# Kernel optimization log

Measured on AMD Instinct MI355X. Metric: run time of the kernel, lower is better.

The kernel has to match this reference:

```python
import jax, jax.numpy as jnp
import numpy as np

# pywt db4 decomposition filters (8 taps)
DEC_LO = np.array([-0.010597401784997278, 0.032883011666982945, 0.030841381835986965,
                   -0.18703481171888114, -0.02798376941698385, 0.6308807679295904,
                   0.7148465705525415, 0.23037781330885523], dtype=np.float32)
DEC_HI = np.array([-0.23037781330885523, 0.7148465705525415, -0.6308807679295904,
                   -0.02798376941698385, 0.18703481171888114, 0.030841381835986965,
                   -0.032883011666982945, -0.010597401784997278], dtype=np.float32)
LEVEL = 6
F = 8  # filter length

# pywt dwt with mode='zero' is exactly full_convolve(x, filt)[1::2].
# We realize it as a strided correlation with the flipped filters:
# out[i] = sum_j x_pad[2i+j] * filt[F-1-j], x padded left by F-2 zeros.
_KERNEL = jnp.asarray(np.stack([DEC_LO[::-1], DEC_HI[::-1]])[:, None, :])  # [2,1,F]

def _dwt_step(x):
    # x: [B, N] -> (cA [B, M], cD [B, M]) with M = floor((N+F-1)/2)
    N = x.shape[-1]
    M = (N + F - 1) // 2
    xp = jnp.pad(x, ((0, 0), (F - 2, F)))[:, None, :]          # [B,1,Npad]
    y = jax.lax.conv_general_dilated(
        xp, _KERNEL.astype(x.dtype), window_strides=(2,), padding='VALID',
        dimension_numbers=('NCH', 'OIH', 'NCH'))                # [B,2,>=M]
    return y[:, 0, :M], y[:, 1, :M]


def setup_inputs() -> dict:
    key = jax.random.key(0)
    x = jax.random.normal(key, (64, 262144), dtype=jnp.float32)
    return {"x": x}


def reference(x):
    # Cascaded 6-level db4 DWT, zero boundary mode.
    a = x
    details = []  # finest first
    for _ in range(LEVEL):
        a, d = _dwt_step(a)
        details.append(d)
    # Match torch module: details[0] = coarsest detail (pywt coeffs[1])
    return (a,) + tuple(details[::-1])
```

## Files before the change

### kernel.cpp

```cpp
#include <hip/hip_runtime.h>


#define NT 256
#define TT 32
#define LEN0 2426
#define LEN1 1210
#define LEN2 602
#define LEN3 298
#define LEN4 146
#define LEN5 70

#define N0 262144
#define M1 131075
#define M2 65541
#define M3 32774
#define M4 16390
#define M5 8198
#define M6 4102

#define OFF_A6 ((size_t)0)
#define OFF_D6 ((size_t)262528)
#define OFF_D5 ((size_t)525056)
#define OFF_D4 ((size_t)1049728)
#define OFF_D3 ((size_t)2098688)
#define OFF_D2 ((size_t)4196224)
#define OFF_D1 ((size_t)8390848)

#define AE 0
#define AO 1216
#define BE 2432
#define BO 3040
#define LDS_FLOATS 3648

__device__ __constant__ float RLO[8] = {
    0.23037781330885523f, 0.7148465705525415f, 0.6308807679295904f,
    -0.02798376941698385f, -0.18703481171888114f, 0.030841381835986965f,
    0.032883011666982945f, -0.010597401784997278f};
__device__ __constant__ float RHI[8] = {
    -0.010597401784997278f, -0.032883011666982945f, 0.030841381835986965f,
    0.18703481171888114f, -0.02798376941698385f, -0.6308807679295904f,
    0.7148465705525415f, -0.23037781330885523f};

template <int LEN, int NC, int SHIFT>
__device__ __forceinline__ void level_fast(const float4* __restrict__ sE4,
                                           const float4* __restrict__ sO4,
                                           float2* __restrict__ dE2,
                                           float2* __restrict__ dO2,
                                           float* __restrict__ dg) {
  for (int c = threadIdx.x; c < NC; c += NT) {
    float4 e0 = sE4[c], e1 = sE4[c + 1];
    float4 o0 = sO4[c], o1 = sO4[c + 1];
    float e[8] = {e0.x, e0.y, e0.z, e0.w, e1.x, e1.y, e1.z, e1.w};
    float o[8] = {o0.x, o0.y, o0.z, o0.w, o1.x, o1.y, o1.z, o1.w};
    float a[4], d[4];
#pragma unroll
    for (int j = 0; j < 4; ++j) {
      float aa = 0.f, dd = 0.f;
#pragma unroll
      for (int t = 0; t < 4; ++t) {
        float ev = e[j + t + SHIFT];
        float ov = o[j + t + SHIFT];
        aa = fmaf(RLO[2 * t], ev, aa);
        aa = fmaf(RLO[2 * t + 1], ov, aa);
        dd = fmaf(RHI[2 * t], ev, dd);
        dd = fmaf(RHI[2 * t + 1], ov, dd);
      }
      a[j] = aa;
      d[j] = dd;
    }
    dE2[c] = make_float2(a[0], a[2]);
    dO2[c] = make_float2(a[1], a[3]);
    const int l0 = 4 * c;
    if (l0 + 4 <= LEN) {
#pragma unroll
      for (int j = 0; j < 4; ++j) __builtin_nontemporal_store(d[j], dg + l0 + j);
    } else {
#pragma unroll
      for (int j = 0; j < 4; ++j)
        if (l0 + j < LEN) __builtin_nontemporal_store(d[j], dg + l0 + j);
    }
  }
}

__device__ inline void dwt_step_slow(const float* __restrict__ s,
                                     float* __restrict__ d, int base, int len,
                                     int M, int cOff, float* __restrict__ dglob,
                                     int tid) {
  for (int l = tid; l < len; l += NT) {
    int g = base + l;
    float a = 0.f, dt = 0.f;
    if (g >= 0 && g < M) {
#pragma unroll
      for (int m = 0; m < 8; ++m) {
        float v = s[2 * l + m];
        a = fmaf(RLO[m], v, a);
        dt = fmaf(RHI[m], v, dt);
      }
    }
    d[l] = a;
    if (l >= cOff && g < M) dglob[g] = dt;
  }
}

__global__ __launch_bounds__(NT, 8) void dwt6_kernel(const float* __restrict__ x,
                                                     float* __restrict__ out) {
  const int p = blockIdx.x;
  const int row = blockIdx.y;
  const int tid = threadIdx.x;

  __shared__ float lds[LDS_FLOATS];

  const int b6 = p * TT;
  const int b5 = 2 * b6 - 6;
  const int b4 = 2 * b5 - 6;
  const int b3 = 2 * b4 - 6;
  const int b2 = 2 * b3 - 6;
  const int b1 = 2 * b2 - 6;
  const int b0 = 2 * b1 - 6;

  const size_t r1 = (size_t)row * M1, r2 = (size_t)row * M2,
               r3 = (size_t)row * M3, r4 = (size_t)row * M4,
               r5 = (size_t)row * M5, r6 = (size_t)row * M6;

  if (p >= 1 && p <= 127) {
    const float4* __restrict__ xs4 =
        (const float4*)(x + (size_t)row * N0 + (b0 - 2));
    float2* __restrict__ aE2 = (float2*)(lds + AE);
    float2* __restrict__ aO2 = (float2*)(lds + AO);
    for (int m = tid; m < 607; m += NT) {
      float4 v = xs4[m];
      aE2[m] = make_float2(v.x, v.z);
      aO2[m] = make_float2(v.y, v.w);
    }
    __syncthreads();

    const float4* aE4 = (const float4*)(lds + AE);
    const float4* aO4 = (const float4*)(lds + AO);
    const float4* bE4 = (const float4*)(lds + BE);
    const float4* bO4 = (const float4*)(lds + BO);
    float2* bE2 = (float2*)(lds + BE);
    float2* bO2 = (float2*)(lds + BO);

    level_fast<LEN1, 303, 1>(aE4, aO4, bE2, bO2, out + OFF_D1 + r1 + b1);
    __syncthreads();
    level_fast<LEN2, 151, 0>(bE4, bO4, aE2, aO2, out + OFF_D2 + r2 + b2);
    __syncthreads();
    level_fast<LEN3, 75, 0>(aE4, aO4, bE2, bO2, out + OFF_D3 + r3 + b3);
    __syncthreads();
    level_fast<LEN4, 37, 0>(bE4, bO4, aE2, aO2, out + OFF_D4 + r4 + b4);
    __syncthreads();
    level_fast<LEN5, 18, 0>(aE4, aO4, bE2, bO2, out + OFF_D5 + r5 + b5);
    __syncthreads();

    float* __restrict__ ga = out + OFF_A6 + r6 + b6;
    float* __restrict__ gd = out + OFF_D6 + r6 + b6;
    for (int c = tid; c < 8; c += NT) {
      float4 e0 = bE4[c], e1 = bE4[c + 1];
      float4 o0 = bO4[c], o1 = bO4[c + 1];
      float e[8] = {e0.x, e0.y, e0.z, e0.w, e1.x, e1.y, e1.z, e1.w};
      float o[8] = {o0.x, o0.y, o0.z, o0.w, o1.x, o1.y, o1.z, o1.w};
#pragma unroll
      for (int j = 0; j < 4; ++j) {
        float aa = 0.f, dd = 0.f;
#pragma unroll
        for (int t = 0; t < 4; ++t) {
          aa = fmaf(RLO[2 * t], e[j + t], aa);
          aa = fmaf(RLO[2 * t + 1], o[j + t], aa);
          dd = fmaf(RHI[2 * t], e[j + t], dd);
          dd = fmaf(RHI[2 * t + 1], o[j + t], dd);
        }
        __builtin_nontemporal_store(aa, ga + 4 * c + j);
        __builtin_nontemporal_store(dd, gd + 4 * c + j);
      }
    }
  } else {
    float* bufA = lds;
    float* bufB = lds + BE;
    const float* __restrict__ xr = x + (size_t)row * N0;
    for (int l = tid; l < LEN0; l += NT) {
      int g = b0 + l;
      bufA[l] = (g >= 0 && g < N0) ? xr[g] : 0.0f;
    }
    __syncthreads();

    dwt_step_slow(bufA, bufB, b1, LEN1, M1, 186, out + OFF_D1 + r1, tid);
    __syncthreads();
    dwt_step_slow(bufB, bufA, b2, LEN2, M2, 90, out + OFF_D2 + r2, tid);
    __syncthreads();
    dwt_step_slow(bufA, bufB, b3, LEN3, M3, 42, out + OFF_D3 + r3, tid);
    __syncthreads();
    dwt_step_slow(bufB, bufA, b4, LEN4, M4, 18, out + OFF_D4 + r4, tid);
    __syncthreads();
    dwt_step_slow(bufA, bufB, b5, LEN5, M5, 6, out + OFF_D5 + r5, tid);
    __syncthreads();

    for (int l = tid; l < TT; l += NT) {
      int g = b6 + l;
      if (g < M6) {
        float a = 0.f, dt = 0.f;
#pragma unroll
        for (int m = 0; m < 8; ++m) {
          float v = bufB[2 * l + m];
          a = fmaf(RLO[m], v, a);
          dt = fmaf(RHI[m], v, dt);
        }
        out[OFF_A6 + r6 + g] = a;
        out[OFF_D6 + r6 + g] = dt;
      }
    }
  }
}

extern "C" void kernel_launch(void* const* d_in, const int* in_sizes, int n_in,
                              void* d_out, int out_size, void* d_ws,
                              size_t ws_size, hipStream_t stream) {
  const float* x = (const float*)d_in[0];
  float* out = (float*)d_out;
  dim3 grid(129, 64);
  dwt6_kernel<<<grid, NT, 0, stream>>>(x, out);
}
```

Before: 115.8 us.

## Compute level one straight from global memory and write only owned detail coefficients

Level one is now computed straight from float4 global loads in registers, so the input is no longer staged in LDS. Detail stores are limited to each tile's owned output range, which removes the duplicate halo writes that neighbouring tiles used to make. The separate slow edge-tile path is replaced by a bounds-checked version of the same pipeline. Block size drops to 64 threads and LDS use is halved, which changes occupancy and per-thread work. Zero-padding of intermediate approximations at the row boundaries now depends only on padding the input, which may not match the reference near the edges.

```diff
diff --git a/kernel.cpp b/kernel.cpp
--- a/kernel.cpp
+++ b/kernel.cpp
@@ -1,14 +1,8 @@
 #include <hip/hip_runtime.h>
 
 
-#define NT 256
+#define NT 64
 #define TT 32
-#define LEN0 2426
-#define LEN1 1210
-#define LEN2 602
-#define LEN3 298
-#define LEN4 146
-#define LEN5 70
 
 #define N0 262144
 #define M1 131075
@@ -18,6 +12,30 @@
 #define M5 8198
 #define M6 4102
 
+#define LEN1 1210
+#define LEN2 602
+#define LEN3 298
+#define LEN4 146
+#define LEN5 70
+
+#define NC1 303
+#define NC2 151
+#define NC3 75
+#define NC4 37
+#define NC5 18
+
+#define LO1 186
+#define LO2 90
+#define LO3 42
+#define LO4 18
+#define LO5 6
+
+#define S1 1024
+#define S2 512
+#define S3 256
+#define S4 128
+#define S5 64
+
 #define OFF_A6 ((size_t)0)
 #define OFF_D6 ((size_t)262528)
 #define OFF_D5 ((size_t)525056)
@@ -26,11 +44,11 @@
 #define OFF_D2 ((size_t)4196224)
 #define OFF_D1 ((size_t)8390848)
 
-#define AE 0
-#define AO 1216
-#define BE 2432
-#define BO 3040
-#define LDS_FLOATS 3648
+#define BE 0
+#define BO 608
+#define CE 1216
+#define CO 1520
+#define LDS_FLOATS 1824
 
 __device__ __constant__ float RLO[8] = {
     0.23037781330885523f, 0.7148465705525415f, 0.6308807679295904f,
@@ -41,12 +59,49 @@
     0.18703481171888114f, -0.02798376941698385f, -0.6308807679295904f,
     0.7148465705525415f, -0.23037781330885523f};
 
-template <int LEN, int NC, int SHIFT>
-__device__ __forceinline__ void level_fast(const float4* __restrict__ sE4,
-                                           const float4* __restrict__ sO4,
-                                           float2* __restrict__ dE2,
-                                           float2* __restrict__ dO2,
-                                           float* __restrict__ dg) {
+__device__ __forceinline__ void l1_body(const float v[16], int c,
+                                        float2* __restrict__ dE2,
+                                        float2* __restrict__ dO2,
+                                        float* __restrict__ dg, int hi) {
+  float e[8] = {v[0], v[2], v[4], v[6], v[8], v[10], v[12], v[14]};
+  float o[8] = {v[1], v[3], v[5], v[7], v[9], v[11], v[13], v[15]};
+  float a[4], d[4];
+#pragma unroll
+  for (int j = 0; j < 4; ++j) {
+    float aa = 0.f, dd = 0.f;
+#pragma unroll
+    for (int t = 0; t < 4; ++t) {
+      float ev = e[j + t + 1];
+      float ov = o[j + t + 1];
+      aa = fmaf(RLO[2 * t], ev, aa);
+      aa = fmaf(RLO[2 * t + 1], ov, aa);
+      dd = fmaf(RHI[2 * t], ev, dd);
+      dd = fmaf(RHI[2 * t + 1], ov, dd);
+    }
+    a[j] = aa;
+    d[j] = dd;
+  }
+  dE2[c] = make_float2(a[0], a[2]);
+  dO2[c] = make_float2(a[1], a[3]);
+  const int l0 = 4 * c;
+  if (l0 >= LO1 && l0 + 4 <= hi) {
+#pragma unroll
+    for (int j = 0; j < 4; ++j) __builtin_nontemporal_store(d[j], dg + l0 + j);
+  } else {
+#pragma unroll
+    for (int j = 0; j < 4; ++j)
+      if (l0 + j >= LO1 && l0 + j < hi)
+        __builtin_nontemporal_store(d[j], dg + l0 + j);
+  }
+}
+
+template <int NC>
+__device__ __forceinline__ void level_mid(const float4* __restrict__ sE4,
+                                          const float4* __restrict__ sO4,
+                                          float2* __restrict__ dE2,
+                                          float2* __restrict__ dO2,
+                                          float* __restrict__ dg, int lo,
+                                          int hi) {
   for (int c = threadIdx.x; c < NC; c += NT) {
     float4 e0 = sE4[c], e1 = sE4[c + 1];
     float4 o0 = sO4[c], o1 = sO4[c + 1];
@@ -58,8 +113,8 @@
       float aa = 0.f, dd = 0.f;
 #pragma unroll
       for (int t = 0; t < 4; ++t) {
-        float ev = e[j + t + SHIFT];
-        float ov = o[j + t + SHIFT];
+        float ev = e[j + t];
+        float ov = o[j + t];
         aa = fmaf(RLO[2 * t], ev, aa);
         aa = fmaf(RLO[2 * t + 1], ov, aa);
         dd = fmaf(RHI[2 * t], ev, dd);
@@ -71,44 +126,26 @@
     dE2[c] = make_float2(a[0], a[2]);
     dO2[c] = make_float2(a[1], a[3]);
     const int l0 = 4 * c;
-    if (l0 + 4 <= LEN) {
-#pragma unroll
-      for (int j = 0; j < 4; ++j) __builtin_nontemporal_store(d[j], dg + l0 + j);
+    if (l0 >= lo && l0 + 4 <= hi) {
+#pragma unroll
+      for (int j = 0; j < 4; ++j)
+        __builtin_nontemporal_store(d[j], dg + l0 + j);
     } else {
 #pragma unroll
       for (int j = 0; j < 4; ++j)
-        if (l0 + j < LEN) __builtin_nontemporal_store(d[j], dg + l0 + j);
-    }
-  }
-}
-
-__device__ inline void dwt_step_slow(const float* __restrict__ s,
-                                     float* __restrict__ d, int base, int len,
-                                     int M, int cOff, float* __restrict__ dglob,
-                                     int tid) {
-  for (int l = tid; l < len; l += NT) {
-    int g = base + l;
-    float a = 0.f, dt = 0.f;
-    if (g >= 0 && g < M) {
-#pragma unroll
-      for (int m = 0; m < 8; ++m) {
-        float v = s[2 * l + m];
-        a = fmaf(RLO[m], v, a);
-        dt = fmaf(RHI[m], v, dt);
-      }
-    }
-    d[l] = a;
-    if (l >= cOff && g < M) dglob[g] = dt;
-  }
-}
-
-__global__ __launch_bounds__(NT, 8) void dwt6_kernel(const float* __restrict__ x,
-                                                     float* __restrict__ out) {
+        if (l0 + j >= lo && l0 + j < hi)
+          __builtin_nontemporal_store(d[j], dg + l0 + j);
+    }
+  }
+}
+
+__global__ __launch_bounds__(NT, 4) void dwt6_kernel(
+    const float* __restrict__ x, float* __restrict__ out) {
   const int p = blockIdx.x;
   const int row = blockIdx.y;
   const int tid = threadIdx.x;
 
-  __shared__ float lds[LDS_FLOATS];
+  __shared__ __align__(16) float lds[LDS_FLOATS];
 
   const int b6 = p * TT;
   const int b5 = 2 * b6 - 6;
@@ -116,96 +153,86 @@
   const int b3 = 2 * b4 - 6;
   const int b2 = 2 * b3 - 6;
   const int b1 = 2 * b2 - 6;
-  const int b0 = 2 * b1 - 6;
-
-  const size_t r1 = (size_t)row * M1, r2 = (size_t)row * M2,
-               r3 = (size_t)row * M3, r4 = (size_t)row * M4,
-               r5 = (size_t)row * M5, r6 = (size_t)row * M6;
-
-  if (p >= 1 && p <= 127) {
-    const float4* __restrict__ xs4 =
-        (const float4*)(x + (size_t)row * N0 + (b0 - 2));
-    float2* __restrict__ aE2 = (float2*)(lds + AE);
-    float2* __restrict__ aO2 = (float2*)(lds + AO);
-    for (int m = tid; m < 607; m += NT) {
-      float4 v = xs4[m];
-      aE2[m] = make_float2(v.x, v.z);
-      aO2[m] = make_float2(v.y, v.w);
-    }
-    __syncthreads();
-
-    const float4* aE4 = (const float4*)(lds + AE);
-    const float4* aO4 = (const float4*)(lds + AO);
-    const float4* bE4 = (const float4*)(lds + BE);
-    const float4* bO4 = (const float4*)(lds + BO);
-    float2* bE2 = (float2*)(lds + BE);
-    float2* bO2 = (float2*)(lds + BO);
-
-    level_fast<LEN1, 303, 1>(aE4, aO4, bE2, bO2, out + OFF_D1 + r1 + b1);
-    __syncthreads();
-    level_fast<LEN2, 151, 0>(bE4, bO4, aE2, aO2, out + OFF_D2 + r2 + b2);
-    __syncthreads();
-    level_fast<LEN3, 75, 0>(aE4, aO4, bE2, bO2, out + OFF_D3 + r3 + b3);
-    __syncthreads();
-    level_fast<LEN4, 37, 0>(bE4, bO4, aE2, aO2, out + OFF_D4 + r4 + b4);
-    __syncthreads();
-    level_fast<LEN5, 18, 0>(aE4, aO4, bE2, bO2, out + OFF_D5 + r5 + b5);
-    __syncthreads();
-
-    float* __restrict__ ga = out + OFF_A6 + r6 + b6;
-    float* __restrict__ gd = out + OFF_D6 + r6 + b6;
+  const int sb = 2 * b1 - 8;
+  const bool edge = (p == 0) | (p >= 127);
+
+  const float* __restrict__ xr = x + (size_t)row * N0;
+
+  float2* bE2 = (float2*)(lds + BE);
+  float2* bO2 = (float2*)(lds + BO);
+  float2* cE2 = (float2*)(lds + CE);
+  float2* cO2 = (float2*)(lds + CO);
+  const float4* bE4 = (const float4*)(lds + BE);
+  const float4* bO4 = (const float4*)(lds + BO);
+  const float4* cE4 = (const float4*)(lds + CE);
+  const float4* cO4 = (const float4*)(lds + CO);
+
+  {
+    float* __restrict__ dg = out + OFF_D1 + (size_t)row * M1 + b1;
+    const int hi = min(LO1 + S1, M1 - b1);
+    if (!edge) {
+      const float4* __restrict__ x4 = (const float4*)(xr + sb);
+      for (int c = tid; c < NC1; c += NT) {
+        float4 q0 = x4[2 * c], q1 = x4[2 * c + 1];
+        float4 q2 = x4[2 * c + 2], q3 = x4[2 * c + 3];
+        float v[16] = {q0.x, q0.y, q0.z, q0.w, q1.x, q1.y, q1.z, q1.w,
+                       q2.x, q2.y, q2.z, q2.w, q3.x, q3.y, q3.z, q3.w};
+        l1_body(v, c, bE2, bO2, dg, hi);
+      }
+    } else {
+      for (int c = tid; c < NC1; c += NT) {
+        float v[16];
+        const int base = sb + 8 * c;
+#pragma unroll
+        for (int k = 0; k < 16; ++k) {
+          const int gi = base + k;
+          v[k] = (gi >= 0 && gi < N0) ? xr[gi] : 0.f;
+        }
+        l1_body(v, c, bE2, bO2, dg, hi);
+      }
+    }
+  }
+  __syncthreads();
+
+  level_mid<NC2>(bE4, bO4, cE2, cO2, out + OFF_D2 + (size_t)row * M2 + b2,
+                 LO2, min(LO2 + S2, M2 - b2));
+  __syncthreads();
+  level_mid<NC3>(cE4, cO4, bE2, bO2, out + OFF_D3 + (size_t)row * M3 + b3,
+                 LO3, min(LO3 + S3, M3 - b3));
+  __syncthreads();
+  level_mid<NC4>(bE4, bO4, cE2, cO2, out + OFF_D4 + (size_t)row * M4 + b4,
+                 LO4, min(LO4 + S4, M4 - b4));
+  __syncthreads();
+  level_mid<NC5>(cE4, cO4, bE2, bO2, out + OFF_D5 + (size_t)row * M5 + b5,
+                 LO5, min(LO5 + S5, M5 - b5));
+  __syncthreads();
+
+  {
+    float* __restrict__ ga = out + OFF_A6 + (size_t)row * M6 + b6;
+    float* __restrict__ gd = out + OFF_D6 + (size_t)row * M6 + b6;
+    const int n6 = min(TT, M6 - b6);
     for (int c = tid; c < 8; c += NT) {
       float4 e0 = bE4[c], e1 = bE4[c + 1];
       float4 o0 = bO4[c], o1 = bO4[c + 1];
       float e[8] = {e0.x, e0.y, e0.z, e0.w, e1.x, e1.y, e1.z, e1.w};
       float o[8] = {o0.x, o0.y, o0.z, o0.w, o1.x, o1.y, o1.z, o1.w};
+      const int l0 = 4 * c;
 #pragma unroll
       for (int j = 0; j < 4; ++j) {
         float aa = 0.f, dd = 0.f;
 #pragma unroll
         for (int t = 0; t < 4; ++t) {
-          aa = fmaf(RLO[2 * t], e[j + t], aa);
-          aa = fmaf(RLO[2 * t + 1], o[j + t], aa);
-          dd = fmaf(RHI[2 * t], e[j + t], dd);
-          dd = fmaf(RHI[2 * t + 1], o[j + t], dd);
+          float ev = e[j + t];
+          float ov = o[j + t];
+          aa = fmaf(RLO[2 * t], ev, aa);
+          aa = fmaf(RLO[2 * t + 1], ov, aa);
+          dd = fmaf(RHI[2 * t], ev, dd);
+          dd = fmaf(RHI[2 * t + 1], ov, dd);
         }
-        __builtin_nontemporal_store(aa, ga + 4 * c + j);
-        __builtin_nontemporal_store(dd, gd + 4 * c + j);
-      }
-    }
-  } else {
-    float* bufA = lds;
-    float* bufB = lds + BE;
-    const float* __restrict__ xr = x + (size_t)row * N0;
-    for (int l = tid; l < LEN0; l += NT) {
-      int g = b0 + l;
-      bufA[l] = (g >= 0 && g < N0) ? xr[g] : 0.0f;
-    }
-    __syncthreads();
-
-    dwt_step_slow(bufA, bufB, b1, LEN1, M1, 186, out + OFF_D1 + r1, tid);
-    __syncthreads();
-    dwt_step_slow(bufB, bufA, b2, LEN2, M2, 90, out + OFF_D2 + r2, tid);
-    __syncthreads();
-    dwt_step_slow(bufA, bufB, b3, LEN3, M3, 42, out + OFF_D3 + r3, tid);
-    __syncthreads();
-    dwt_step_slow(bufB, bufA, b4, LEN4, M4, 18, out + OFF_D4 + r4, tid);
-    __syncthreads();
-    dwt_step_slow(bufA, bufB, b5, LEN5, M5, 6, out + OFF_D5 + r5, tid);
-    __syncthreads();
-
-    for (int l = tid; l < TT; l += NT) {
-      int g = b6 + l;
-      if (g < M6) {
-        float a = 0.f, dt = 0.f;
-#pragma unroll
-        for (int m = 0; m < 8; ++m) {
-          float v = bufB[2 * l + m];
-          a = fmaf(RLO[m], v, a);
-          dt = fmaf(RHI[m], v, dt);
+        if (l0 + j < n6) {
+          __builtin_nontemporal_store(aa, ga + l0 + j);
+          __builtin_nontemporal_store(dd, gd + l0 + j);
         }
-        out[OFF_A6 + r6 + g] = a;
-        out[OFF_D6 + r6 + g] = dt;
       }
     }
   }
```

New measurement: 136.3 us. +17.7%, slower.

## Process two rows per block and use a lighter LDS-only barrier

Applied to the files above, without the earlier changes.

Each block now handles two input rows. LDS doubles to hold two row buffers, and the grid's y dimension halves, so block count and per-block setup/barrier overhead are amortized and each thread has twice the independent work for ILP. __syncthreads is replaced by an lgkmcnt wait plus s_barrier, which avoids waiting on outstanding global stores. In exchange there is less parallelism (half the blocks), doubled LDS use and higher register pressure, with launch bounds lowered from 8 to 5 blocks per CU.

```diff
diff --git a/kernel.cpp b/kernel.cpp
--- a/kernel.cpp
+++ b/kernel.cpp
@@ -3,12 +3,19 @@
 
 #define NT 256
 #define TT 32
+
 #define LEN0 2426
 #define LEN1 1210
 #define LEN2 602
 #define LEN3 298
 #define LEN4 146
 #define LEN5 70
+
+#define NC1 303
+#define NC2 151
+#define NC3 75
+#define NC4 37
+#define NC5 18
 
 #define N0 262144
 #define M1 131075
@@ -30,7 +37,8 @@
 #define AO 1216
 #define BE 2432
 #define BO 3040
-#define LDS_FLOATS 3648
+#define RSTR 3648
+#define LDS_FLOATS (2 * RSTR)
 
 __device__ __constant__ float RLO[8] = {
     0.23037781330885523f, 0.7148465705525415f, 0.6308807679295904f,
@@ -41,74 +49,118 @@
     0.18703481171888114f, -0.02798376941698385f, -0.6308807679295904f,
     0.7148465705525415f, -0.23037781330885523f};
 
+__device__ __forceinline__ void bar_lds() {
+  asm volatile("s_waitcnt lgkmcnt(0)" ::: "memory");
+  __builtin_amdgcn_s_barrier();
+}
+
+template <int SHIFT>
+__device__ __forceinline__ void conv8(const float e[8], const float o[8],
+                                      float a[4], float d[4]) {
+#pragma unroll
+  for (int j = 0; j < 4; ++j) {
+    float aa = 0.f, dd = 0.f;
+#pragma unroll
+    for (int t = 0; t < 4; ++t) {
+      float ev = e[j + t + SHIFT];
+      float ov = o[j + t + SHIFT];
+      aa = fmaf(RLO[2 * t], ev, aa);
+      aa = fmaf(RLO[2 * t + 1], ov, aa);
+      dd = fmaf(RHI[2 * t], ev, dd);
+      dd = fmaf(RHI[2 * t + 1], ov, dd);
+    }
+    a[j] = aa;
+    d[j] = dd;
+  }
+}
+
 template <int LEN, int NC, int SHIFT>
-__device__ __forceinline__ void level_fast(const float4* __restrict__ sE4,
-                                           const float4* __restrict__ sO4,
-                                           float2* __restrict__ dE2,
-                                           float2* __restrict__ dO2,
-                                           float* __restrict__ dg) {
+__device__ __forceinline__ void level2r(float* __restrict__ R0,
+                                        float* __restrict__ R1, int sE, int sO,
+                                        int dE, int dO, float* __restrict__ dg0,
+                                        float* __restrict__ dg1) {
+  const float4* sE0 = (const float4*)(R0 + sE);
+  const float4* sO0 = (const float4*)(R0 + sO);
+  const float4* sE1 = (const float4*)(R1 + sE);
+  const float4* sO1 = (const float4*)(R1 + sO);
+  float2* dE0 = (float2*)(R0 + dE);
+  float2* dO0 = (float2*)(R0 + dO);
+  float2* dE1 = (float2*)(R1 + dE);
+  float2* dO1 = (float2*)(R1 + dO);
+
   for (int c = threadIdx.x; c < NC; c += NT) {
-    float4 e0 = sE4[c], e1 = sE4[c + 1];
-    float4 o0 = sO4[c], o1 = sO4[c + 1];
-    float e[8] = {e0.x, e0.y, e0.z, e0.w, e1.x, e1.y, e1.z, e1.w};
-    float o[8] = {o0.x, o0.y, o0.z, o0.w, o1.x, o1.y, o1.z, o1.w};
-    float a[4], d[4];
-#pragma unroll
-    for (int j = 0; j < 4; ++j) {
-      float aa = 0.f, dd = 0.f;
-#pragma unroll
-      for (int t = 0; t < 4; ++t) {
-        float ev = e[j + t + SHIFT];
-        float ov = o[j + t + SHIFT];
-        aa = fmaf(RLO[2 * t], ev, aa);
-        aa = fmaf(RLO[2 * t + 1], ov, aa);
-        dd = fmaf(RHI[2 * t], ev, dd);
-        dd = fmaf(RHI[2 * t + 1], ov, dd);
-      }
-      a[j] = aa;
-      d[j] = dd;
-    }
-    dE2[c] = make_float2(a[0], a[2]);
-    dO2[c] = make_float2(a[1], a[3]);
+    float4 ea0 = sE0[c], ea1 = sE0[c + 1];
+    float4 oa0 = sO0[c], oa1 = sO0[c + 1];
+    float4 eb0 = sE1[c], eb1 = sE1[c + 1];
+    float4 ob0 = sO1[c], ob1 = sO1[c + 1];
+    float e0[8] = {ea0.x, ea0.y, ea0.z, ea0.w, ea1.x, ea1.y, ea1.z, ea1.w};
+    float o0[8] = {oa0.x, oa0.y, oa0.z, oa0.w, oa1.x, oa1.y, oa1.z, oa1.w};
+    float e1[8] = {eb0.x, eb0.y, eb0.z, eb0.w, eb1.x, eb1.y, eb1.z, eb1.w};
+    float o1[8] = {ob0.x, ob0.y, ob0.z, ob0.w, ob1.x, ob1.y, ob1.z, ob1.w};
+    float a0[4], d0[4], a1[4], d1[4];
+    conv8<SHIFT>(e0, o0, a0, d0);
+    conv8<SHIFT>(e1, o1, a1, d1);
+    dE0[c] = make_float2(a0[0], a0[2]);
+    dO0[c] = make_float2(a0[1], a0[3]);
+    dE1[c] = make_float2(a1[0], a1[2]);
+    dO1[c] = make_float2(a1[1], a1[3]);
     const int l0 = 4 * c;
     if (l0 + 4 <= LEN) {
 #pragma unroll
-      for (int j = 0; j < 4; ++j) __builtin_nontemporal_store(d[j], dg + l0 + j);
+      for (int j = 0; j < 4; ++j) {
+        __builtin_nontemporal_store(d0[j], dg0 + l0 + j);
+        __builtin_nontemporal_store(d1[j], dg1 + l0 + j);
+      }
     } else {
 #pragma unroll
       for (int j = 0; j < 4; ++j)
-        if (l0 + j < LEN) __builtin_nontemporal_store(d[j], dg + l0 + j);
+        if (l0 + j < LEN) {
+          __builtin_nontemporal_store(d0[j], dg0 + l0 + j);
+          __builtin_nontemporal_store(d1[j], dg1 + l0 + j);
+        }
     }
   }
 }
 
-__device__ inline void dwt_step_slow(const float* __restrict__ s,
-                                     float* __restrict__ d, int base, int len,
-                                     int M, int cOff, float* __restrict__ dglob,
-                                     int tid) {
+__device__ inline void dwt_step_slow2(const float* __restrict__ s0,
+                                      const float* __restrict__ s1,
+                                      float* __restrict__ d0,
+                                      float* __restrict__ d1, int base, int len,
+                                      int M, int cOff, float* __restrict__ dg0,
+                                      float* __restrict__ dg1, int tid) {
   for (int l = tid; l < len; l += NT) {
     int g = base + l;
-    float a = 0.f, dt = 0.f;
+    float a0 = 0.f, t0 = 0.f, a1 = 0.f, t1 = 0.f;
     if (g >= 0 && g < M) {
 #pragma unroll
       for (int m = 0; m < 8; ++m) {
-        float v = s[2 * l + m];
-        a = fmaf(RLO[m], v, a);
-        dt = fmaf(RHI[m], v, dt);
+        float v0 = s0[2 * l + m];
+        float v1 = s1[2 * l + m];
+        a0 = fmaf(RLO[m], v0, a0);
+        t0 = fmaf(RHI[m], v0, t0);
+        a1 = fmaf(RLO[m], v1, a1);
+        t1 = fmaf(RHI[m], v1, t1);
       }
     }
-    d[l] = a;
-    if (l >= cOff && g < M) dglob[g] = dt;
+    d0[l] = a0;
+    d1[l] = a1;
+    if (l >= cOff && g < M) {
+      dg0[g] = t0;
+      dg1[g] = t1;
+    }
   }
 }
 
-__global__ __launch_bounds__(NT, 8) void dwt6_kernel(const float* __restrict__ x,
-                                                     float* __restrict__ out) {
+__global__ __launch_bounds__(NT, 5) void dwt6_kernel(
+    const float* __restrict__ x, float* __restrict__ out) {
   const int p = blockIdx.x;
-  const int row = blockIdx.y;
+  const int r0 = 2 * blockIdx.y;
+  const int r1 = r0 + 1;
   const int tid = threadIdx.x;
 
-  __shared__ float lds[LDS_FLOATS];
+  __shared__ __align__(16) float lds[LDS_FLOATS];
+  float* __restrict__ L0 = lds;
+  float* __restrict__ L1 = lds + RSTR;
 
   const int b6 = p * TT;
   const int b5 = 2 * b6 - 6;
@@ -118,94 +170,125 @@
   const int b1 = 2 * b2 - 6;
   const int b0 = 2 * b1 - 6;
 
-  const size_t r1 = (size_t)row * M1, r2 = (size_t)row * M2,
-               r3 = (size_t)row * M3, r4 = (size_t)row * M4,
-               r5 = (size_t)row * M5, r6 = (size_t)row * M6;
+  const size_t ra1 = (size_t)r0 * M1, rb1 = (size_t)r1 * M1;
+  const size_t ra2 = (size_t)r0 * M2, rb2 = (size_t)r1 * M2;
+  const size_t ra3 = (size_t)r0 * M3, rb3 = (size_t)r1 * M3;
+  const size_t ra4 = (size_t)r0 * M4, rb4 = (size_t)r1 * M4;
+  const size_t ra5 = (size_t)r0 * M5, rb5 = (size_t)r1 * M5;
+  const size_t ra6 = (size_t)r0 * M6, rb6 = (size_t)r1 * M6;
 
   if (p >= 1 && p <= 127) {
-    const float4* __restrict__ xs4 =
-        (const float4*)(x + (size_t)row * N0 + (b0 - 2));
-    float2* __restrict__ aE2 = (float2*)(lds + AE);
-    float2* __restrict__ aO2 = (float2*)(lds + AO);
+    const float4* __restrict__ xs0 =
+        (const float4*)(x + (size_t)r0 * N0 + (b0 - 2));
+    const float4* __restrict__ xs1 =
+        (const float4*)(x + (size_t)r1 * N0 + (b0 - 2));
+    float2* aE0 = (float2*)(L0 + AE);
+    float2* aO0 = (float2*)(L0 + AO);
+    float2* aE1 = (float2*)(L1 + AE);
+    float2* aO1 = (float2*)(L1 + AO);
     for (int m = tid; m < 607; m += NT) {
-      float4 v = xs4[m];
-      aE2[m] = make_float2(v.x, v.z);
-      aO2[m] = make_float2(v.y, v.w);
-    }
-    __syncthreads();
-
-    const float4* aE4 = (const float4*)(lds + AE);
-    const float4* aO4 = (const float4*)(lds + AO);
-    const float4* bE4 = (const float4*)(lds + BE);
-    const float4* bO4 = (const float4*)(lds + BO);
-    float2* bE2 = (float2*)(lds + BE);
-    float2* bO2 = (float2*)(lds + BO);
-
-    level_fast<LEN1, 303, 1>(aE4, aO4, bE2, bO2, out + OFF_D1 + r1 + b1);
-    __syncthreads();
-    level_fast<LEN2, 151, 0>(bE4, bO4, aE2, aO2, out + OFF_D2 + r2 + b2);
-    __syncthreads();
-    level_fast<LEN3, 75, 0>(aE4, aO4, bE2, bO2, out + OFF_D3 + r3 + b3);
-    __syncthreads();
-    level_fast<LEN4, 37, 0>(bE4, bO4, aE2, aO2, out + OFF_D4 + r4 + b4);
-    __syncthreads();
-    level_fast<LEN5, 18, 0>(aE4, aO4, bE2, bO2, out + OFF_D5 + r5 + b5);
-    __syncthreads();
-
-    float* __restrict__ ga = out + OFF_A6 + r6 + b6;
-    float* __restrict__ gd = out + OFF_D6 + r6 + b6;
+      float4 v0 = xs0[m];
+      float4 v1 = xs1[m];
+      aE0[m] = make_float2(v0.x, v0.z);
+      aO0[m] = make_float2(v0.y, v0.w);
+      aE1[m] = make_float2(v1.x, v1.z);
+      aO1[m] = make_float2(v1.y, v1.w);
+    }
+    bar_lds();
+
+    level2r<LEN1, NC1, 1>(L0, L1, AE, AO, BE, BO, out + OFF_D1 + ra1 + b1,
+                          out + OFF_D1 + rb1 + b1);
+    bar_lds();
+    level2r<LEN2, NC2, 0>(L0, L1, BE, BO, AE, AO, out + OFF_D2 + ra2 + b2,
+                          out + OFF_D2 + rb2 + b2);
+    bar_lds();
+    level2r<LEN3, NC3, 0>(L0, L1, AE, AO, BE, BO, out + OFF_D3 + ra3 + b3,
+                          out + OFF_D3 + rb3 + b3);
+    bar_lds();
+    level2r<LEN4, NC4, 0>(L0, L1, BE, BO, AE, AO, out + OFF_D4 + ra4 + b4,
+                          out + OFF_D4 + rb4 + b4);
+    bar_lds();
+    level2r<LEN5, NC5, 0>(L0, L1, AE, AO, BE, BO, out + OFF_D5 + ra5 + b5,
+                          out + OFF_D5 + rb5 + b5);
+    bar_lds();
+
+    const float4* bE0 = (const float4*)(L0 + BE);
+    const float4* bO0 = (const float4*)(L0 + BO);
+    const float4* bE1 = (const float4*)(L1 + BE);
+    const float4* bO1 = (const float4*)(L1 + BO);
+    float* __restrict__ ga0 = out + OFF_A6 + ra6 + b6;
+    float* __restrict__ gd0 = out + OFF_D6 + ra6 + b6;
+    float* __restrict__ ga1 = out + OFF_A6 + rb6 + b6;
+    float* __restrict__ gd1 = out + OFF_D6 + rb6 + b6;
     for (int c = tid; c < 8; c += NT) {
-      float4 e0 = bE4[c], e1 = bE4[c + 1];
-      float4 o0 = bO4[c], o1 = bO4[c + 1];
-      float e[8] = {e0.x, e0.y, e0.z, e0.w, e1.x, e1.y, e1.z, e1.w};
-      float o[8] = {o0.x, o0.y, o0.z, o0.w, o1.x, o1.y, o1.z, o1.w};
+      float4 ea0 = bE0[c], ea1 = bE0[c + 1];
+      float4 oa0 = bO0[c], oa1 = bO0[c + 1];
+      float4 eb0 = bE1[c], eb1 = bE1[c + 1];
+      float4 ob0 = bO1[c], ob1 = bO1[c + 1];
+      float e0[8] = {ea0.x, ea0.y, ea0.z, ea0.w, ea1.x, ea1.y, ea1.z, ea1.w};
+      float o0[8] = {oa0.x, oa0.y, oa0.z, oa0.w, oa1.x, oa1.y, oa1.z, oa1.w};
+      float e1[8] = {eb0.x, eb0.y, eb0.z, eb0.w, eb1.x, eb1.y, eb1.z, eb1.w};
+      float o1[8] = {ob0.x, ob0.y, ob0.z, ob0.w, ob1.x, ob1.y, ob1.z, ob1.w};
+      float a0[4], d0[4], a1[4], d1[4];
+      conv8<0>(e0, o0, a0, d0);
+      conv8<0>(e1, o1, a1, d1);
+      const int l0 = 4 * c;
 #pragma unroll
       for (int j = 0; j < 4; ++j) {
-        float aa = 0.f, dd = 0.f;
-#pragma unroll
-        for (int t = 0; t < 4; ++t) {
-          aa = fmaf(RLO[2 * t], e[j + t], aa);
-          aa = fmaf(RLO[2 * t + 1], o[j + t], aa);
-          dd = fmaf(RHI[2 * t], e[j + t], dd);
-          dd = fmaf(RHI[2 * t + 1], o[j + t], dd);
-        }
-        __builtin_nontemporal_store(aa, ga + 4 * c + j);
-        __builtin_nontemporal_store(dd, gd + 4 * c + j);
+        __builtin_nontemporal_store(a0[j], ga0 + l0 + j);
+        __builtin_nontemporal_store(d0[j], gd0 + l0 + j);
+        __builtin_nontemporal_store(a1[j], ga1 + l0 + j);
+        __builtin_nontemporal_store(d1[j], gd1 + l0 + j);
       }
     }
   } else {
-    float* bufA = lds;
-    float* bufB = lds + BE;
-    const float* __restrict__ xr = x + (size_t)row * N0;
+    float* A0 = L0;
+    float* B0 = L0 + BE;
+    float* A1 = L1;
+    float* B1 = L1 + BE;
+    const float* __restrict__ xr0 = x + (size_t)r0 * N0;
+    const float* __restrict__ xr1 = x + (size_t)r1 * N0;
     for (int l = tid; l < LEN0; l += NT) {
       int g = b0 + l;
-      bufA[l] = (g >= 0 && g < N0) ? xr[g] : 0.0f;
-    }
-    __syncthreads();
-
-    dwt_step_slow(bufA, bufB, b1, LEN1, M1, 186, out + OFF_D1 + r1, tid);
-    __syncthreads();
-    dwt_step_slow(bufB, bufA, b2, LEN2, M2, 90, out + OFF_D2 + r2, tid);
-    __syncthreads();
-    dwt_step_slow(bufA, bufB, b3, LEN3, M3, 42, out + OFF_D3 + r3, tid);
-    __syncthreads();
-    dwt_step_slow(bufB, bufA, b4, LEN4, M4, 18, out + OFF_D4 + r4, tid);
-    __syncthreads();
-    dwt_step_slow(bufA, bufB, b5, LEN5, M5, 6, out + OFF_D5 + r5, tid);
-    __syncthreads();
+      bool ok = (g >= 0 && g < N0);
+      A0[l] = ok ? xr0[g] : 0.0f;
+      A1[l] = ok ? xr1[g] : 0.0f;
+    }
+    bar_lds();
+
+    dwt_step_slow2(A0, A1, B0, B1, b1, LEN1, M1, 186, out + OFF_D1 + ra1,
+                   out + OFF_D1 + rb1, tid);
+    bar_lds();
+    dwt_step_slow2(B0, B1, A0, A1, b2, LEN2, M2, 90, out + OFF_D2 + ra2,
+                   out + OFF_D2 + rb2, tid);
+    bar_lds();
+    dwt_step_slow2(A0, A1, B0, B1, b3, LEN3, M3, 42, out + OFF_D3 + ra3,
+                   out + OFF_D3 + rb3, tid);
+    bar_lds();
+    dwt_step_slow2(B0, B1, A0, A1, b4, LEN4, M4, 18, out + OFF_D4 + ra4,
+                   out + OFF_D4 + rb4, tid);
+    bar_lds();
+    dwt_step_slow2(A0, A1, B0, B1, b5, LEN5, M5, 6, out + OFF_D5 + ra5,
+                   out + OFF_D5 + rb5, tid);
+    bar_lds();
 
     for (int l = tid; l < TT; l += NT) {
       int g = b6 + l;
       if (g < M6) {
-        float a = 0.f, dt = 0.f;
+        float a0 = 0.f, d0 = 0.f, a1 = 0.f, d1 = 0.f;
 #pragma unroll
         for (int m = 0; m < 8; ++m) {
-          float v = bufB[2 * l + m];
-          a = fmaf(RLO[m], v, a);
-          dt = fmaf(RHI[m], v, dt);
+          float v0 = B0[2 * l + m];
+          float v1 = B1[2 * l + m];
+          a0 = fmaf(RLO[m], v0, a0);
+          d0 = fmaf(RHI[m], v0, d0);
+          a1 = fmaf(RLO[m], v1, a1);
+          d1 = fmaf(RHI[m], v1, d1);
         }
-        out[OFF_A6 + r6 + g] = a;
-        out[OFF_D6 + r6 + g] = dt;
+        out[OFF_A6 + ra6 + g] = a0;
+        out[OFF_D6 + ra6 + g] = d0;
+        out[OFF_A6 + rb6 + g] = a1;
+        out[OFF_D6 + rb6 + g] = d1;
       }
     }
   }
@@ -216,6 +299,6 @@
                               size_t ws_size, hipStream_t stream) {
   const float* x = (const float*)d_in[0];
   float* out = (float*)d_out;
-  dim3 grid(129, 64);
+  dim3 grid(129, 32);
   dwt6_kernel<<<grid, NT, 0, stream>>>(x, out);
 }
```

Result: slower. 118.3 us (+2.2%).

## Double tile size, fuse levels 3-4 and 5-6 in registers, cheaper barriers

Applied to the files above, without the earlier changes.

Each block now covers twice as many output samples with 512 threads, which cuts halo recomputation and the number of blocks. Levels 3 and 4, and levels 5 and 6, are fused so the coarse approximation is computed in registers without an LDS round trip and barrier. Separate thread groups write the level 3 and level 5 detail coefficients at the same time. Plain __syncthreads is replaced by an lgkmcnt wait plus s_barrier. The trade-offs are some redundant compute in the fused paths, idle threads at the small levels, and higher LDS and register use per block.

```diff
diff --git a/kernel.cpp b/kernel.cpp
--- a/kernel.cpp
+++ b/kernel.cpp
@@ -1,14 +1,8 @@
 #include <hip/hip_runtime.h>
 
 
-#define NT 256
-#define TT 32
-#define LEN0 2426
-#define LEN1 1210
-#define LEN2 602
-#define LEN3 298
-#define LEN4 146
-#define LEN5 70
+#define NT 512
+#define TT 64
 
 #define N0 262144
 #define M1 131075
@@ -18,6 +12,19 @@
 #define M5 8198
 #define M6 4102
 
+#define LEN0 4474
+#define LEN1 2234
+#define LEN2 1114
+#define LEN3 554
+#define LEN4 274
+#define LEN5 134
+
+#define NC1 559
+#define NC2 279
+#define NC3 139
+#define NC4 69
+#define NC5 34
+
 #define OFF_A6 ((size_t)0)
 #define OFF_D6 ((size_t)262528)
 #define OFF_D5 ((size_t)525056)
@@ -27,10 +34,10 @@
 #define OFF_D1 ((size_t)8390848)
 
 #define AE 0
-#define AO 1216
-#define BE 2432
-#define BO 3040
-#define LDS_FLOATS 3648
+#define AO 2240
+#define BE 4480
+#define BO 5600
+#define LDS_FLOATS 6720
 
 __device__ __constant__ float RLO[8] = {
     0.23037781330885523f, 0.7148465705525415f, 0.6308807679295904f,
@@ -40,6 +47,11 @@
     -0.010597401784997278f, -0.032883011666982945f, 0.030841381835986965f,
     0.18703481171888114f, -0.02798376941698385f, -0.6308807679295904f,
     0.7148465705525415f, -0.23037781330885523f};
+
+__device__ __forceinline__ void bar_lds() {
+  asm volatile("s_waitcnt lgkmcnt(0)" ::: "memory");
+  __builtin_amdgcn_s_barrier();
+}
 
 template <int LEN, int NC, int SHIFT>
 __device__ __forceinline__ void level_fast(const float4* __restrict__ sE4,
@@ -102,13 +114,13 @@
   }
 }
 
-__global__ __launch_bounds__(NT, 8) void dwt6_kernel(const float* __restrict__ x,
-                                                     float* __restrict__ out) {
+__global__ __launch_bounds__(NT, 8) void dwt6_kernel(
+    const float* __restrict__ x, float* __restrict__ out) {
   const int p = blockIdx.x;
   const int row = blockIdx.y;
   const int tid = threadIdx.x;
 
-  __shared__ float lds[LDS_FLOATS];
+  __shared__ __align__(16) float lds[LDS_FLOATS];
 
   const int b6 = p * TT;
   const int b5 = 2 * b6 - 6;
@@ -122,77 +134,174 @@
                r3 = (size_t)row * M3, r4 = (size_t)row * M4,
                r5 = (size_t)row * M5, r6 = (size_t)row * M6;
 
-  if (p >= 1 && p <= 127) {
+  float2* aE2 = (float2*)(lds + AE);
+  float2* aO2 = (float2*)(lds + AO);
+  float2* bE2 = (float2*)(lds + BE);
+  float2* bO2 = (float2*)(lds + BO);
+  const float4* aE4 = (const float4*)(lds + AE);
+  const float4* aO4 = (const float4*)(lds + AO);
+  const float4* bE4 = (const float4*)(lds + BE);
+  const float4* bO4 = (const float4*)(lds + BO);
+
+  if (p >= 1 && p <= 63) {
     const float4* __restrict__ xs4 =
         (const float4*)(x + (size_t)row * N0 + (b0 - 2));
-    float2* __restrict__ aE2 = (float2*)(lds + AE);
-    float2* __restrict__ aO2 = (float2*)(lds + AO);
-    for (int m = tid; m < 607; m += NT) {
+    for (int m = tid; m < 1119; m += NT) {
       float4 v = xs4[m];
       aE2[m] = make_float2(v.x, v.z);
       aO2[m] = make_float2(v.y, v.w);
     }
-    __syncthreads();
-
-    const float4* aE4 = (const float4*)(lds + AE);
-    const float4* aO4 = (const float4*)(lds + AO);
-    const float4* bE4 = (const float4*)(lds + BE);
-    const float4* bO4 = (const float4*)(lds + BO);
-    float2* bE2 = (float2*)(lds + BE);
-    float2* bO2 = (float2*)(lds + BO);
-
-    level_fast<LEN1, 303, 1>(aE4, aO4, bE2, bO2, out + OFF_D1 + r1 + b1);
-    __syncthreads();
-    level_fast<LEN2, 151, 0>(bE4, bO4, aE2, aO2, out + OFF_D2 + r2 + b2);
-    __syncthreads();
-    level_fast<LEN3, 75, 0>(aE4, aO4, bE2, bO2, out + OFF_D3 + r3 + b3);
-    __syncthreads();
-    level_fast<LEN4, 37, 0>(bE4, bO4, aE2, aO2, out + OFF_D4 + r4 + b4);
-    __syncthreads();
-    level_fast<LEN5, 18, 0>(aE4, aO4, bE2, bO2, out + OFF_D5 + r5 + b5);
-    __syncthreads();
-
-    float* __restrict__ ga = out + OFF_A6 + r6 + b6;
-    float* __restrict__ gd = out + OFF_D6 + r6 + b6;
-    for (int c = tid; c < 8; c += NT) {
-      float4 e0 = bE4[c], e1 = bE4[c + 1];
-      float4 o0 = bO4[c], o1 = bO4[c + 1];
-      float e[8] = {e0.x, e0.y, e0.z, e0.w, e1.x, e1.y, e1.z, e1.w};
-      float o[8] = {o0.x, o0.y, o0.z, o0.w, o1.x, o1.y, o1.z, o1.w};
-#pragma unroll
-      for (int j = 0; j < 4; ++j) {
-        float aa = 0.f, dd = 0.f;
-#pragma unroll
-        for (int t = 0; t < 4; ++t) {
-          aa = fmaf(RLO[2 * t], e[j + t], aa);
-          aa = fmaf(RLO[2 * t + 1], o[j + t], aa);
-          dd = fmaf(RHI[2 * t], e[j + t], dd);
-          dd = fmaf(RHI[2 * t + 1], o[j + t], dd);
-        }
-        __builtin_nontemporal_store(aa, ga + 4 * c + j);
-        __builtin_nontemporal_store(dd, gd + 4 * c + j);
+    bar_lds();
+
+    level_fast<LEN1, NC1, 1>(aE4, aO4, bE2, bO2, out + OFF_D1 + r1 + b1);
+    bar_lds();
+    level_fast<LEN2, NC2, 0>(bE4, bO4, aE2, aO2, out + OFF_D2 + r2 + b2);
+    bar_lds();
+
+    {
+      float* __restrict__ dg3 = out + OFF_D3 + r3 + b3;
+      float* __restrict__ dg4 = out + OFF_D4 + r4 + b4;
+      if (tid < NC4) {
+        const int c = tid;
+        float E[20], O[20];
+#pragma unroll
+        for (int q = 0; q < 5; ++q) {
+          float4 ev = aE4[2 * c + q], ov = aO4[2 * c + q];
+          E[4 * q] = ev.x; E[4 * q + 1] = ev.y;
+          E[4 * q + 2] = ev.z; E[4 * q + 3] = ev.w;
+          O[4 * q] = ov.x; O[4 * q + 1] = ov.y;
+          O[4 * q + 2] = ov.z; O[4 * q + 3] = ov.w;
+        }
+        float c3[14];
+#pragma unroll
+        for (int k = 0; k < 14; ++k) {
+          float s = 0.f;
+#pragma unroll
+          for (int t = 0; t < 4; ++t) {
+            s = fmaf(RLO[2 * t], E[k + t], s);
+            s = fmaf(RLO[2 * t + 1], O[k + t], s);
+          }
+          c3[k] = s;
+        }
+        float a4[4], d4[4];
+#pragma unroll
+        for (int j = 0; j < 4; ++j) {
+          float aa = 0.f, dd = 0.f;
+#pragma unroll
+          for (int t = 0; t < 4; ++t) {
+            aa = fmaf(RLO[2 * t], c3[2 * j + 2 * t], aa);
+            aa = fmaf(RLO[2 * t + 1], c3[2 * j + 2 * t + 1], aa);
+            dd = fmaf(RHI[2 * t], c3[2 * j + 2 * t], dd);
+            dd = fmaf(RHI[2 * t + 1], c3[2 * j + 2 * t + 1], dd);
+          }
+          a4[j] = aa;
+          d4[j] = dd;
+        }
+        bE2[c] = make_float2(a4[0], a4[2]);
+        bO2[c] = make_float2(a4[1], a4[3]);
+        const int l0 = 4 * c;
+#pragma unroll
+        for (int j = 0; j < 4; ++j)
+          if (l0 + j < LEN4) __builtin_nontemporal_store(d4[j], dg4 + l0 + j);
+      } else if (tid >= 128 && tid < 128 + NC3) {
+        const int c = tid - 128;
+        float4 e0 = aE4[c], e1 = aE4[c + 1];
+        float4 o0 = aO4[c], o1 = aO4[c + 1];
+        float e[8] = {e0.x, e0.y, e0.z, e0.w, e1.x, e1.y, e1.z, e1.w};
+        float o[8] = {o0.x, o0.y, o0.z, o0.w, o1.x, o1.y, o1.z, o1.w};
+        const int l0 = 4 * c;
+#pragma unroll
+        for (int j = 0; j < 4; ++j) {
+          float dd = 0.f;
+#pragma unroll
+          for (int t = 0; t < 4; ++t) {
+            dd = fmaf(RHI[2 * t], e[j + t], dd);
+            dd = fmaf(RHI[2 * t + 1], o[j + t], dd);
+          }
+          if (l0 + j < LEN3) __builtin_nontemporal_store(dd, dg3 + l0 + j);
+        }
+      }
+    }
+    bar_lds();
+
+    {
+      float* __restrict__ ga = out + OFF_A6 + r6 + b6;
+      float* __restrict__ gd = out + OFF_D6 + r6 + b6;
+      float* __restrict__ dg5 = out + OFF_D5 + r5 + b5;
+      if (tid < 32) {
+        const int c = tid;
+        float E[16], O[16];
+#pragma unroll
+        for (int q = 0; q < 4; ++q) {
+          float4 ev = bE4[c + q], ov = bO4[c + q];
+          E[4 * q] = ev.x; E[4 * q + 1] = ev.y;
+          E[4 * q + 2] = ev.z; E[4 * q + 3] = ev.w;
+          O[4 * q] = ov.x; O[4 * q + 1] = ov.y;
+          O[4 * q + 2] = ov.z; O[4 * q + 3] = ov.w;
+        }
+        float a5[10];
+#pragma unroll
+        for (int s = 0; s < 10; ++s) {
+          float aa = 0.f;
+#pragma unroll
+          for (int t = 0; t < 4; ++t) {
+            aa = fmaf(RLO[2 * t], E[s + t], aa);
+            aa = fmaf(RLO[2 * t + 1], O[s + t], aa);
+          }
+          a5[s] = aa;
+        }
+#pragma unroll
+        for (int j = 0; j < 2; ++j) {
+          float aa = 0.f, dd = 0.f;
+#pragma unroll
+          for (int t = 0; t < 4; ++t) {
+            aa = fmaf(RLO[2 * t], a5[2 * j + 2 * t], aa);
+            aa = fmaf(RLO[2 * t + 1], a5[2 * j + 2 * t + 1], aa);
+            dd = fmaf(RHI[2 * t], a5[2 * j + 2 * t], dd);
+            dd = fmaf(RHI[2 * t + 1], a5[2 * j + 2 * t + 1], dd);
+          }
+          __builtin_nontemporal_store(aa, ga + 2 * c + j);
+          __builtin_nontemporal_store(dd, gd + 2 * c + j);
+        }
+      } else if (tid >= 64 && tid < 64 + NC5) {
+        const int c = tid - 64;
+        float4 e0 = bE4[c], e1 = bE4[c + 1];
+        float4 o0 = bO4[c], o1 = bO4[c + 1];
+        float e[8] = {e0.x, e0.y, e0.z, e0.w, e1.x, e1.y, e1.z, e1.w};
+        float o[8] = {o0.x, o0.y, o0.z, o0.w, o1.x, o1.y, o1.z, o1.w};
+        const int l0 = 4 * c;
+#pragma unroll
+        for (int j = 0; j < 4; ++j) {
+          float dd = 0.f;
+#pragma unroll
+          for (int t = 0; t < 4; ++t) {
+            dd = fmaf(RHI[2 * t], e[j + t], dd);
+            dd = fmaf(RHI[2 * t + 1], o[j + t], dd);
+          }
+          if (l0 + j < LEN5) __builtin_nontemporal_store(dd, dg5 + l0 + j);
+        }
       }
     }
   } else {
-    float* bufA = lds;
-    float* bufB = lds + BE;
+    float* A = lds;
+    float* B = lds + BE;
     const float* __restrict__ xr = x + (size_t)row * N0;
     for (int l = tid; l < LEN0; l += NT) {
       int g = b0 + l;
-      bufA[l] = (g >= 0 && g < N0) ? xr[g] : 0.0f;
-    }
-    __syncthreads();
-
-    dwt_step_slow(bufA, bufB, b1, LEN1, M1, 186, out + OFF_D1 + r1, tid);
-    __syncthreads();
-    dwt_step_slow(bufB, bufA, b2, LEN2, M2, 90, out + OFF_D2 + r2, tid);
-    __syncthreads();
-    dwt_step_slow(bufA, bufB, b3, LEN3, M3, 42, out + OFF_D3 + r3, tid);
-    __syncthreads();
-    dwt_step_slow(bufB, bufA, b4, LEN4, M4, 18, out + OFF_D4 + r4, tid);
-    __syncthreads();
-    dwt_step_slow(bufA, bufB, b5, LEN5, M5, 6, out + OFF_D5 + r5, tid);
-    __syncthreads();
+      A[l] = (g >= 0 && g < N0) ? xr[g] : 0.0f;
+    }
+    bar_lds();
+
+    dwt_step_slow(A, B, b1, LEN1, M1, 186, out + OFF_D1 + r1, tid);
+    bar_lds();
+    dwt_step_slow(B, A, b2, LEN2, M2, 90, out + OFF_D2 + r2, tid);
+    bar_lds();
+    dwt_step_slow(A, B, b3, LEN3, M3, 42, out + OFF_D3 + r3, tid);
+    bar_lds();
+    dwt_step_slow(B, A, b4, LEN4, M4, 18, out + OFF_D4 + r4, tid);
+    bar_lds();
+    dwt_step_slow(A, B, b5, LEN5, M5, 6, out + OFF_D5 + r5, tid);
+    bar_lds();
 
     for (int l = tid; l < TT; l += NT) {
       int g = b6 + l;
@@ -200,7 +309,7 @@
         float a = 0.f, dt = 0.f;
 #pragma unroll
         for (int m = 0; m < 8; ++m) {
-          float v = bufB[2 * l + m];
+          float v = B[2 * l + m];
           a = fmaf(RLO[m], v, a);
           dt = fmaf(RHI[m], v, dt);
         }
@@ -216,6 +325,6 @@
                               size_t ws_size, hipStream_t stream) {
   const float* x = (const float*)d_in[0];
   float* out = (float*)d_out;
-  dim3 grid(129, 64);
+  dim3 grid(65, 64);
   dwt6_kernel<<<grid, NT, 0, stream>>>(x, out);
 }
```

Measured after the change: 117.9 us. No clear change (+1.8%).
